# Kernel tuning notes

Hardware: AMD Instinct MI355X
Metric: run time of the kernel (lower is better)

Reference implementation:

```python
import jax, jax.numpy as jnp
import numpy as np

N = 50000      # nodes
E = 800000     # edges (avg degree 16)
D_IN = 128
HID = 128
OUT = 64


def setup_inputs() -> dict:
    key = jax.random.key(0)
    ks = jax.random.split(key, 10)
    s = 0.05
    return {
        "node_feats": jax.random.normal(ks[0], (N, D_IN), jnp.float32),
        "edge_index": jax.random.randint(ks[1], (2, E), 0, N, jnp.int32),
        "W1": jax.random.normal(ks[2], (D_IN, HID), jnp.float32) * s,
        "b1": jnp.zeros((HID,), jnp.float32),
        "W2": jax.random.normal(ks[3], (HID, HID), jnp.float32) * s,
        "b2": jnp.zeros((HID,), jnp.float32),
        "W3": jax.random.normal(ks[4], (HID, OUT), jnp.float32) * s,
        "b3": jnp.zeros((OUT,), jnp.float32),
        "skip_W": jax.random.normal(ks[5], (HID, OUT), jnp.float32) * s,
        "skip_b": jnp.zeros((OUT,), jnp.float32),
    }


def _gcn(h, src, dst, out_norm, in_norm, W, b):
    # DGL GraphConv, norm='both': scale src by out_deg^-1/2, sum over incoming
    # edges at dst, scale by in_deg^-1/2, then linear transform + bias.
    h = h * out_norm[:, None]                                   # [N, d]
    agg = jax.ops.segment_sum(h[src], dst, num_segments=N)      # [N, d]
    return (agg * in_norm[:, None]) @ W + b


def reference(node_feats, edge_index, W1, b1, W2, b2, W3, b3, skip_W, skip_b):
    src, dst = edge_index[0], edge_index[1]
    ones = jnp.ones((E,), jnp.float32)
    out_deg = jax.ops.segment_sum(ones, src, num_segments=N)
    in_deg = jax.ops.segment_sum(ones, dst, num_segments=N)
    out_norm = jnp.maximum(out_deg, 1.0) ** -0.5
    in_norm = jnp.maximum(in_deg, 1.0) ** -0.5

    # layer 0 (no skip) + ReLU
    h = jax.nn.relu(_gcn(node_feats, src, dst, out_norm, in_norm, W1, b1))
    # layer 1: same-dim residual blend + ReLU
    g2 = _gcn(h, src, dst, out_norm, in_norm, W2, b2)
    h = jax.nn.relu(0.6 * h + 0.4 * g2)
    # layer 2 (last, no ReLU): dims differ -> projected skip blend
    g3 = _gcn(h, src, dst, out_norm, in_norm, W3, b3)
    h = 0.6 * (h @ skip_W + skip_b) + 0.4 * g3
    return h[None]  # [1, N, OUT]
```

## Files before the change

kernel.cpp:

```cpp
#include <hip/hip_runtime.h>
#include <hip/hip_fp16.h>
#include <math.h>

#define TPB 256
#define CAP 64

__global__ __launch_bounds__(TPB) void k_count(const int* __restrict__ ei, int E,
                                               int* __restrict__ cnt, int* __restrict__ od,
                                               unsigned short* __restrict__ slots) {
    int t = blockIdx.x * TPB + threadIdx.x;
    int base = t * 4;
    if (base + 3 < E) {
        int4 s4 = *(const int4*)(ei + base);
        int4 d4 = *(const int4*)(ei + E + base);
        int p0 = atomicAdd(&cnt[d4.x], 1);
        int p1 = atomicAdd(&cnt[d4.y], 1);
        int p2 = atomicAdd(&cnt[d4.z], 1);
        int p3 = atomicAdd(&cnt[d4.w], 1);
        atomicAdd(&od[s4.x], 1);
        atomicAdd(&od[s4.y], 1);
        atomicAdd(&od[s4.z], 1);
        atomicAdd(&od[s4.w], 1);
        if (p0 < CAP) slots[(d4.x << 6) + p0] = (unsigned short)s4.x;
        if (p1 < CAP) slots[(d4.y << 6) + p1] = (unsigned short)s4.y;
        if (p2 < CAP) slots[(d4.z << 6) + p2] = (unsigned short)s4.z;
        if (p3 < CAP) slots[(d4.w << 6) + p3] = (unsigned short)s4.w;
    } else {
        for (int e = base; e < E; ++e) {
            int s = ei[e], d = ei[E + e];
            int pos = atomicAdd(&cnt[d], 1);
            if (pos < CAP) slots[(d << 6) + pos] = (unsigned short)s;
            atomicAdd(&od[s], 1);
        }
    }
}

__global__ __launch_bounds__(TPB) void k_norm(const int* __restrict__ od, const int* __restrict__ cnt,
                                              float* __restrict__ onr, float* __restrict__ rsq,
                                              float* __restrict__ inr, int N) {
    int i = blockIdx.x * TPB + threadIdx.x;
    if (i < N) {
        float o = fmaxf((float)od[i], 1.0f);
        float q = sqrtf(o);
        onr[i] = 1.0f / q;
        rsq[i] = q;
        inr[i] = 1.0f / sqrtf(fmaxf((float)cnt[i], 1.0f));
    }
}

__global__ __launch_bounds__(TPB) void k_cvt(const float* __restrict__ x, const float* __restrict__ onr,
                                             __half2* __restrict__ xh, int nF4) {
    int i4 = blockIdx.x * TPB + threadIdx.x;
    if (i4 >= nF4) return;
    int row = i4 >> 5;
    float on = onr[row];
    float4 v = ((const float4*)x)[i4];
    __half2 a = __floats2half2_rn(v.x * on, v.y * on);
    __half2 b = __floats2half2_rn(v.z * on, v.w * on);
    uint2 u;
    u.x = *reinterpret_cast<unsigned int*>(&a);
    u.y = *reinterpret_cast<unsigned int*>(&b);
    ((uint2*)xh)[i4] = u;
}

__global__ __launch_bounds__(TPB) void k_spmmh(const __half2* __restrict__ hp,
                                               const int* __restrict__ cnt,
                                               const unsigned short* __restrict__ slots,
                                               const float* __restrict__ inr,
                                               float* __restrict__ agg, int N) {
    int lane = threadIdx.x & 63;
    int r = blockIdx.x * 4 + (threadIdx.x >> 6);
    if (r >= N) return;
    int n = cnt[r]; if (n > CAP) n = CAP;
    const unsigned short* sl = slots + (r << 6);
    float ax0 = 0.f, ay0 = 0.f, ax1 = 0.f, ay1 = 0.f;
    float ax2 = 0.f, ay2 = 0.f, ax3 = 0.f, ay3 = 0.f;
    int e = 0;
    for (; e + 7 < n; e += 8) {
        ushort4 qa = *(const ushort4*)(sl + e);
        ushort4 qb = *(const ushort4*)(sl + e + 4);
        __half2 v0 = hp[qa.x * 64 + lane];
        __half2 v1 = hp[qa.y * 64 + lane];
        __half2 v2 = hp[qa.z * 64 + lane];
        __half2 v3 = hp[qa.w * 64 + lane];
        __half2 v4 = hp[qb.x * 64 + lane];
        __half2 v5 = hp[qb.y * 64 + lane];
        __half2 v6 = hp[qb.z * 64 + lane];
        __half2 v7 = hp[qb.w * 64 + lane];
        float2 f0 = __half22float2(v0), f1 = __half22float2(v1);
        float2 f2 = __half22float2(v2), f3 = __half22float2(v3);
        float2 f4 = __half22float2(v4), f5 = __half22float2(v5);
        float2 f6 = __half22float2(v6), f7 = __half22float2(v7);
        ax0 += f0.x + f1.x;  ay0 += f0.y + f1.y;
        ax1 += f2.x + f3.x;  ay1 += f2.y + f3.y;
        ax2 += f4.x + f5.x;  ay2 += f4.y + f5.y;
        ax3 += f6.x + f7.x;  ay3 += f6.y + f7.y;
    }
    for (; e + 3 < n; e += 4) {
        ushort4 qa = *(const ushort4*)(sl + e);
        float2 f0 = __half22float2(hp[qa.x * 64 + lane]);
        float2 f1 = __half22float2(hp[qa.y * 64 + lane]);
        float2 f2 = __half22float2(hp[qa.z * 64 + lane]);
        float2 f3 = __half22float2(hp[qa.w * 64 + lane]);
        ax0 += f0.x + f1.x;  ay0 += f0.y + f1.y;
        ax1 += f2.x + f3.x;  ay1 += f2.y + f3.y;
    }
    for (; e < n; ++e) {
        float2 f0 = __half22float2(hp[sl[e] * 64 + lane]);
        ax0 += f0.x;  ay0 += f0.y;
    }
    float sc = inr[r];
    float2 o;
    o.x = sc * ((ax0 + ax1) + (ax2 + ax3));
    o.y = sc * ((ay0 + ay1) + (ay2 + ay3));
    ((float2*)agg)[r * 64 + lane] = o;
}

__global__ __launch_bounds__(TPB) void k_spmm_final(const float* __restrict__ Pskip,
                                                    const __half* __restrict__ Ph,
                                                    const int* __restrict__ cnt,
                                                    const unsigned short* __restrict__ slots,
                                                    const float* __restrict__ inr,
                                                    const float* __restrict__ b3, const float* __restrict__ bs,
                                                    float* __restrict__ out, int N) {
    int lane = threadIdx.x & 63;
    int r = blockIdx.x * 4 + (threadIdx.x >> 6);
    if (r >= N) return;
    int n = cnt[r]; if (n > CAP) n = CAP;
    const unsigned short* sl = slots + (r << 6);
    float a0 = 0.f, a1 = 0.f, a2 = 0.f, a3 = 0.f;
    float a4 = 0.f, a5 = 0.f, a6 = 0.f, a7 = 0.f;
    int e = 0;
    for (; e + 7 < n; e += 8) {
        ushort4 qa = *(const ushort4*)(sl + e);
        ushort4 qb = *(const ushort4*)(sl + e + 4);
        a0 += __half2float(Ph[qa.x * 64 + lane]);
        a1 += __half2float(Ph[qa.y * 64 + lane]);
        a2 += __half2float(Ph[qa.z * 64 + lane]);
        a3 += __half2float(Ph[qa.w * 64 + lane]);
        a4 += __half2float(Ph[qb.x * 64 + lane]);
        a5 += __half2float(Ph[qb.y * 64 + lane]);
        a6 += __half2float(Ph[qb.z * 64 + lane]);
        a7 += __half2float(Ph[qb.w * 64 + lane]);
    }
    for (; e + 3 < n; e += 4) {
        ushort4 qa = *(const ushort4*)(sl + e);
        a0 += __half2float(Ph[qa.x * 64 + lane]);
        a1 += __half2float(Ph[qa.y * 64 + lane]);
        a2 += __half2float(Ph[qa.z * 64 + lane]);
        a3 += __half2float(Ph[qa.w * 64 + lane]);
    }
    for (; e < n; ++e) a0 += __half2float(Ph[sl[e] * 64 + lane]);
    float g3 = inr[r] * (((a0 + a1) + (a2 + a3)) + ((a4 + a5) + (a6 + a7))) + b3[lane];
    float skip = Pskip[r * 64 + lane] + bs[lane];
    out[r * 64 + lane] = 0.6f * skip + 0.4f * g3;
}

template <int MODE>
__global__ __launch_bounds__(TPB) void k_gemm(const float* __restrict__ A,
                                              const float* __restrict__ Wa, const float* __restrict__ Wb,
                                              const float* __restrict__ bias, const float* __restrict__ H,
                                              const float* __restrict__ onr, const float* __restrict__ rsq,
                                              float* __restrict__ C, __half* __restrict__ Ch, int N) {
    __shared__ float As[64][132];
    int t = threadIdx.x;
    int bm = blockIdx.x * 64;
#pragma unroll
    for (int rep = 0; rep < 8; ++rep) {
        int idx = rep * TPB + t;
        int i = idx >> 5;
        int k4 = (idx & 31) * 4;
        int row = bm + i;
        float4 v = make_float4(0.f, 0.f, 0.f, 0.f);
        if (row < N) {
            v = *(const float4*)(&A[row * 128 + k4]);
            if (MODE == 2) {
                float rs = rsq[row];
                v.x *= rs; v.y *= rs; v.z *= rs; v.w *= rs;
            }
        }
        *(float4*)(&As[i][k4]) = v;
    }
    __syncthreads();
    int tx = t & 31, ty = t >> 5;
    int j0 = tx * 4;
    const float* Wp;
    int jj, ldw;
    if (MODE == 2) { Wp = (j0 < 64) ? Wa : Wb; jj = j0 & 63; ldw = 64; }
    else           { Wp = Wa;                   jj = j0;      ldw = 128; }
    float4 acc[8];
#pragma unroll
    for (int q = 0; q < 8; ++q) acc[q] = make_float4(0.f, 0.f, 0.f, 0.f);
    for (int k = 0; k < 128; k += 4) {
        float4 w0 = *(const float4*)(&Wp[(k + 0) * ldw + jj]);
        float4 w1 = *(const float4*)(&Wp[(k + 1) * ldw + jj]);
        float4 w2 = *(const float4*)(&Wp[(k + 2) * ldw + jj]);
        float4 w3 = *(const float4*)(&Wp[(k + 3) * ldw + jj]);
#pragma unroll
        for (int q = 0; q < 8; ++q) {
            float4 a = *(const float4*)(&As[ty + 8 * q][k]);
            acc[q].x += a.x * w0.x + a.y * w1.x + a.z * w2.x + a.w * w3.x;
            acc[q].y += a.x * w0.y + a.y * w1.y + a.z * w2.y + a.w * w3.y;
            acc[q].z += a.x * w0.z + a.y * w1.z + a.z * w2.z + a.w * w3.z;
            acc[q].w += a.x * w0.w + a.y * w1.w + a.z * w2.w + a.w * w3.w;
        }
    }
    float4 bv = make_float4(0.f, 0.f, 0.f, 0.f);
    if (MODE != 2) bv = *(const float4*)(&bias[j0]);
#pragma unroll
    for (int q = 0; q < 8; ++q) {
        int row = bm + ty + 8 * q;
        if (row >= N) continue;
        float4 o;
        o.x = acc[q].x + bv.x;
        o.y = acc[q].y + bv.y;
        o.z = acc[q].z + bv.z;
        o.w = acc[q].w + bv.w;
        if (MODE == 1) {
            float hs = rsq[row];
            float4 h = *(const float4*)(&H[row * 128 + j0]);
            o.x = 0.6f * h.x * hs + 0.4f * o.x;
            o.y = 0.6f * h.y * hs + 0.4f * o.y;
            o.z = 0.6f * h.z * hs + 0.4f * o.z;
            o.w = 0.6f * h.w * hs + 0.4f * o.w;
        }
        if (MODE != 2) {
            float on = onr[row];
            o.x = fmaxf(o.x, 0.f) * on;
            o.y = fmaxf(o.y, 0.f) * on;
            o.z = fmaxf(o.z, 0.f) * on;
            o.w = fmaxf(o.w, 0.f) * on;
            *(float4*)(&C[row * 128 + j0]) = o;
            if (MODE == 0) {
                __half2 ha = __floats2half2_rn(o.x, o.y);
                __half2 hb = __floats2half2_rn(o.z, o.w);
                uint2 u;
                u.x = *reinterpret_cast<unsigned int*>(&ha);
                u.y = *reinterpret_cast<unsigned int*>(&hb);
                *(uint2*)(&Ch[row * 128 + j0]) = u;
            }
        } else {
            if (j0 < 64) {
                *(float4*)(&C[row * 64 + j0]) = o;
            } else {
                float on = onr[row];
                __half2 ha = __floats2half2_rn(o.x * on, o.y * on);
                __half2 hb = __floats2half2_rn(o.z * on, o.w * on);
                uint2 u;
                u.x = *reinterpret_cast<unsigned int*>(&ha);
                u.y = *reinterpret_cast<unsigned int*>(&hb);
                *(uint2*)(&Ch[row * 64 + (j0 - 64)]) = u;
            }
        }
    }
}

extern "C" void kernel_launch(void* const* d_in, const int* in_sizes, int n_in,
                              void* d_out, int out_size, void* d_ws, size_t ws_size,
                              hipStream_t stream) {
    const float* x  = (const float*)d_in[0];
    const int*   ei = (const int*)d_in[1];
    const float* W1 = (const float*)d_in[2];
    const float* b1 = (const float*)d_in[3];
    const float* W2 = (const float*)d_in[4];
    const float* b2 = (const float*)d_in[5];
    const float* W3 = (const float*)d_in[6];
    const float* b3 = (const float*)d_in[7];
    const float* Ws = (const float*)d_in[8];
    const float* bs = (const float*)d_in[9];
    float* out = (float*)d_out;

    int N = in_sizes[0] / 128;
    int E = in_sizes[1] / 2;

    char* p = (char*)d_ws;
    auto alloc = [&](size_t bytes) -> char* {
        char* r = p;
        p += (bytes + 255) & ~(size_t)255;
        return r;
    };
    size_t npad = ((size_t)N * 4 + 255) & ~(size_t)255;
    int*   cnt  = (int*)alloc(npad);
    int*   od   = (int*)alloc(npad);
    float* onr  = (float*)alloc((size_t)N * 4);
    float* rsq  = (float*)alloc((size_t)N * 4);
    float* inr  = (float*)alloc((size_t)N * 4);
    unsigned short* slots = (unsigned short*)alloc((size_t)N * CAP * 2);
    __half* xh  = (__half*)alloc((size_t)N * 128 * 2);
    float* agg  = (float*)alloc((size_t)N * 128 * 4);
    float* h1s  = (float*)alloc((size_t)N * 128 * 4);
    float* h2s  = (float*)alloc((size_t)N * 128 * 4);
    (void)ws_size; (void)n_in; (void)out_size;

    __half* h1h   = xh;
    float*  Pskip = agg;
    __half* Ph    = (__half*)(agg + (size_t)N * 64);

    int cBlocks = ((E + 3) / 4 + TPB - 1) / TPB;
    int nBlocks = (N + TPB - 1) / TPB;
    int cvtBlocks = (N * 32 + TPB - 1) / TPB;
    int spmmBlocks = (N + 3) / 4;
    int gemmBlocks = (N + 63) / 64;

    hipMemsetAsync(cnt, 0, npad * 2, stream);

    k_count<<<cBlocks, TPB, 0, stream>>>(ei, E, cnt, od, slots);
    k_norm<<<nBlocks, TPB, 0, stream>>>(od, cnt, onr, rsq, inr, N);
    k_cvt<<<cvtBlocks, TPB, 0, stream>>>(x, onr, (__half2*)xh, N * 32);

    k_spmmh<<<spmmBlocks, TPB, 0, stream>>>((const __half2*)xh, cnt, slots, inr, agg, N);
    k_gemm<0><<<gemmBlocks, TPB, 0, stream>>>(agg, W1, nullptr, b1, nullptr, onr, rsq, h1s, h1h, N);
    k_spmmh<<<spmmBlocks, TPB, 0, stream>>>((const __half2*)h1h, cnt, slots, inr, agg, N);
    k_gemm<1><<<gemmBlocks, TPB, 0, stream>>>(agg, W2, nullptr, b2, h1s, onr, rsq, h2s, nullptr, N);
    k_gemm<2><<<gemmBlocks, TPB, 0, stream>>>(h2s, Ws, W3, nullptr, nullptr, onr, rsq, Pskip, Ph, N);
    k_spmm_final<<<spmmBlocks, TPB, 0, stream>>>(Pskip, Ph, cnt, slots, inr, b3, bs, out, N);
}
```

Measured before the change: 376.4 us.

## Switch dense GEMMs to fp16 MFMA and store aggregates in half precision

Replaces the three fp32 FMA-based dense GEMMs with fp16 MFMA 16x16x32 instructions, using weights pre-transposed and converted to half by a new small kernel. The SpMM now writes its aggregate in half precision and layer-two activations are kept only in half, which halves intermediate memory traffic. The rsq rescaling path is removed in favour of storing unscaled fp32 h1 for the residual. This lowers GEMM compute and bandwidth costs but adds fp16 rounding on aggregates and activations.

Measured after the change: 334.5 us. -11.1%, faster.

```diff
diff --git a/kernel.cpp b/kernel.cpp
--- a/kernel.cpp
+++ b/kernel.cpp
@@ -4,6 +4,9 @@
 
 #define TPB 256
 #define CAP 64
+
+typedef _Float16 f16x8 __attribute__((ext_vector_type(8)));
+typedef float f32x4 __attribute__((ext_vector_type(4)));
 
 __global__ __launch_bounds__(TPB) void k_count(const int* __restrict__ ei, int E,
                                                int* __restrict__ cnt, int* __restrict__ od,
@@ -36,16 +39,28 @@
 }
 
 __global__ __launch_bounds__(TPB) void k_norm(const int* __restrict__ od, const int* __restrict__ cnt,
-                                              float* __restrict__ onr, float* __restrict__ rsq,
-                                              float* __restrict__ inr, int N) {
+                                              float* __restrict__ onr, float* __restrict__ inr, int N) {
     int i = blockIdx.x * TPB + threadIdx.x;
     if (i < N) {
-        float o = fmaxf((float)od[i], 1.0f);
-        float q = sqrtf(o);
-        onr[i] = 1.0f / q;
-        rsq[i] = q;
+        onr[i] = 1.0f / sqrtf(fmaxf((float)od[i], 1.0f));
         inr[i] = 1.0f / sqrtf(fmaxf((float)cnt[i], 1.0f));
     }
+}
+
+__global__ __launch_bounds__(TPB) void k_cvtw(const float* __restrict__ W1, const float* __restrict__ W2,
+                                              const float* __restrict__ Ws, const float* __restrict__ W3,
+                                              __half* __restrict__ W1T, __half* __restrict__ W2T,
+                                              __half* __restrict__ WCT) {
+    int idx = blockIdx.x * TPB + threadIdx.x;
+    int m = idx >> 14;
+    int r = idx & 16383;
+    int j = r >> 7, k = r & 127;
+    float v;
+    __half* dst;
+    if (m == 0)      { v = W1[k * 128 + j]; dst = W1T; }
+    else if (m == 1) { v = W2[k * 128 + j]; dst = W2T; }
+    else             { v = (j < 64) ? Ws[k * 64 + j] : W3[k * 64 + (j - 64)]; dst = WCT; }
+    dst[r] = __float2half(v);
 }
 
 __global__ __launch_bounds__(TPB) void k_cvt(const float* __restrict__ x, const float* __restrict__ onr,
@@ -67,7 +82,7 @@
                                                const int* __restrict__ cnt,
                                                const unsigned short* __restrict__ slots,
                                                const float* __restrict__ inr,
-                                               float* __restrict__ agg, int N) {
+                                               __half2* __restrict__ aggh, int N) {
     int lane = threadIdx.x & 63;
     int r = blockIdx.x * 4 + (threadIdx.x >> 6);
     if (r >= N) return;
@@ -79,18 +94,14 @@
     for (; e + 7 < n; e += 8) {
         ushort4 qa = *(const ushort4*)(sl + e);
         ushort4 qb = *(const ushort4*)(sl + e + 4);
-        __half2 v0 = hp[qa.x * 64 + lane];
-        __half2 v1 = hp[qa.y * 64 + lane];
-        __half2 v2 = hp[qa.z * 64 + lane];
-        __half2 v3 = hp[qa.w * 64 + lane];
-        __half2 v4 = hp[qb.x * 64 + lane];
-        __half2 v5 = hp[qb.y * 64 + lane];
-        __half2 v6 = hp[qb.z * 64 + lane];
-        __half2 v7 = hp[qb.w * 64 + lane];
-        float2 f0 = __half22float2(v0), f1 = __half22float2(v1);
-        float2 f2 = __half22float2(v2), f3 = __half22float2(v3);
-        float2 f4 = __half22float2(v4), f5 = __half22float2(v5);
-        float2 f6 = __half22float2(v6), f7 = __half22float2(v7);
+        float2 f0 = __half22float2(hp[qa.x * 64 + lane]);
+        float2 f1 = __half22float2(hp[qa.y * 64 + lane]);
+        float2 f2 = __half22float2(hp[qa.z * 64 + lane]);
+        float2 f3 = __half22float2(hp[qa.w * 64 + lane]);
+        float2 f4 = __half22float2(hp[qb.x * 64 + lane]);
+        float2 f5 = __half22float2(hp[qb.y * 64 + lane]);
+        float2 f6 = __half22float2(hp[qb.z * 64 + lane]);
+        float2 f7 = __half22float2(hp[qb.w * 64 + lane]);
         ax0 += f0.x + f1.x;  ay0 += f0.y + f1.y;
         ax1 += f2.x + f3.x;  ay1 += f2.y + f3.y;
         ax2 += f4.x + f5.x;  ay2 += f4.y + f5.y;
@@ -110,10 +121,8 @@
         ax0 += f0.x;  ay0 += f0.y;
     }
     float sc = inr[r];
-    float2 o;
-    o.x = sc * ((ax0 + ax1) + (ax2 + ax3));
-    o.y = sc * ((ay0 + ay1) + (ay2 + ay3));
-    ((float2*)agg)[r * 64 + lane] = o;
+    aggh[r * 64 + lane] =
+        __floats2half2_rn(sc * ((ax0 + ax1) + (ax2 + ax3)), sc * ((ay0 + ay1) + (ay2 + ay3)));
 }
 
 __global__ __launch_bounds__(TPB) void k_spmm_final(const float* __restrict__ Pskip,
@@ -157,99 +166,74 @@
 }
 
 template <int MODE>
-__global__ __launch_bounds__(TPB) void k_gemm(const float* __restrict__ A,
-                                              const float* __restrict__ Wa, const float* __restrict__ Wb,
-                                              const float* __restrict__ bias, const float* __restrict__ H,
-                                              const float* __restrict__ onr, const float* __restrict__ rsq,
-                                              float* __restrict__ C, __half* __restrict__ Ch, int N) {
-    __shared__ float As[64][132];
+__global__ __launch_bounds__(TPB) void k_mgemm(const __half* __restrict__ Ah,
+                                               const __half* __restrict__ WT,
+                                               const float* __restrict__ bias,
+                                               const float* __restrict__ Hres,
+                                               const float* __restrict__ onr,
+                                               float* __restrict__ Cf, __half* __restrict__ Chh,
+                                               int N) {
+    __shared__ _Float16 As[64][136];
     int t = threadIdx.x;
     int bm = blockIdx.x * 64;
 #pragma unroll
-    for (int rep = 0; rep < 8; ++rep) {
-        int idx = rep * TPB + t;
-        int i = idx >> 5;
-        int k4 = (idx & 31) * 4;
-        int row = bm + i;
-        float4 v = make_float4(0.f, 0.f, 0.f, 0.f);
-        if (row < N) {
-            v = *(const float4*)(&A[row * 128 + k4]);
-            if (MODE == 2) {
-                float rs = rsq[row];
-                v.x *= rs; v.y *= rs; v.z *= rs; v.w *= rs;
-            }
+    for (int rep = 0; rep < 4; ++rep) {
+        int c = rep * TPB + t;
+        int row = c >> 4, cc = c & 15;
+        int grow = bm + row;
+        f16x8 v = {0, 0, 0, 0, 0, 0, 0, 0};
+        if (grow < N) v = *(const f16x8*)(Ah + (size_t)grow * 128 + cc * 8);
+        *(f16x8*)(&As[row][cc * 8]) = v;
+    }
+    __syncthreads();
+    int l = t & 63;
+    int w = t >> 6;
+    int wrow = w * 16;
+    int lr = l & 15;
+    int lk = (l >> 4) * 8;
+    f32x4 acc[8];
+    f32x4 zero = {0.f, 0.f, 0.f, 0.f};
+#pragma unroll
+    for (int j = 0; j < 8; ++j) acc[j] = zero;
+#pragma unroll
+    for (int kk = 0; kk < 4; ++kk) {
+        f16x8 af = *(const f16x8*)(&As[wrow + lr][kk * 32 + lk]);
+#pragma unroll
+        for (int jt = 0; jt < 8; ++jt) {
+            f16x8 bf = *(const f16x8*)(WT + (size_t)(jt * 16 + lr) * 128 + kk * 32 + lk);
+            acc[jt] = __builtin_amdgcn_mfma_f32_16x16x32_f16(af, bf, acc[jt], 0, 0, 0);
         }
-        *(float4*)(&As[i][k4]) = v;
-    }
-    __syncthreads();
-    int tx = t & 31, ty = t >> 5;
-    int j0 = tx * 4;
-    const float* Wp;
-    int jj, ldw;
-    if (MODE == 2) { Wp = (j0 < 64) ? Wa : Wb; jj = j0 & 63; ldw = 64; }
-    else           { Wp = Wa;                   jj = j0;      ldw = 128; }
-    float4 acc[8];
-#pragma unroll
-    for (int q = 0; q < 8; ++q) acc[q] = make_float4(0.f, 0.f, 0.f, 0.f);
-    for (int k = 0; k < 128; k += 4) {
-        float4 w0 = *(const float4*)(&Wp[(k + 0) * ldw + jj]);
-        float4 w1 = *(const float4*)(&Wp[(k + 1) * ldw + jj]);
-        float4 w2 = *(const float4*)(&Wp[(k + 2) * ldw + jj]);
-        float4 w3 = *(const float4*)(&Wp[(k + 3) * ldw + jj]);
-#pragma unroll
-        for (int q = 0; q < 8; ++q) {
-            float4 a = *(const float4*)(&As[ty + 8 * q][k]);
-            acc[q].x += a.x * w0.x + a.y * w1.x + a.z * w2.x + a.w * w3.x;
-            acc[q].y += a.x * w0.y + a.y * w1.y + a.z * w2.y + a.w * w3.y;
-            acc[q].z += a.x * w0.z + a.y * w1.z + a.z * w2.z + a.w * w3.z;
-            acc[q].w += a.x * w0.w + a.y * w1.w + a.z * w2.w + a.w * w3.w;
+    }
+    int r0 = (l >> 4) * 4;
+    float onr4[4];
+    if (MODE == 0 || MODE == 2) {
+#pragma unroll
+        for (int r = 0; r < 4; ++r) {
+            int row = bm + wrow + r0 + r;
+            onr4[r] = (row < N) ? onr[row] : 0.f;
         }
     }
-    float4 bv = make_float4(0.f, 0.f, 0.f, 0.f);
-    if (MODE != 2) bv = *(const float4*)(&bias[j0]);
-#pragma unroll
-    for (int q = 0; q < 8; ++q) {
-        int row = bm + ty + 8 * q;
-        if (row >= N) continue;
-        float4 o;
-        o.x = acc[q].x + bv.x;
-        o.y = acc[q].y + bv.y;
-        o.z = acc[q].z + bv.z;
-        o.w = acc[q].w + bv.w;
-        if (MODE == 1) {
-            float hs = rsq[row];
-            float4 h = *(const float4*)(&H[row * 128 + j0]);
-            o.x = 0.6f * h.x * hs + 0.4f * o.x;
-            o.y = 0.6f * h.y * hs + 0.4f * o.y;
-            o.z = 0.6f * h.z * hs + 0.4f * o.z;
-            o.w = 0.6f * h.w * hs + 0.4f * o.w;
-        }
-        if (MODE != 2) {
-            float on = onr[row];
-            o.x = fmaxf(o.x, 0.f) * on;
-            o.y = fmaxf(o.y, 0.f) * on;
-            o.z = fmaxf(o.z, 0.f) * on;
-            o.w = fmaxf(o.w, 0.f) * on;
-            *(float4*)(&C[row * 128 + j0]) = o;
+#pragma unroll
+    for (int jt = 0; jt < 8; ++jt) {
+        int col = jt * 16 + lr;
+        float bv = 0.f;
+        if (MODE != 2) bv = bias[col];
+#pragma unroll
+        for (int r = 0; r < 4; ++r) {
+            int row = bm + wrow + r0 + r;
+            if (row >= N) continue;
+            float v = acc[jt][r] + bv;
             if (MODE == 0) {
-                __half2 ha = __floats2half2_rn(o.x, o.y);
-                __half2 hb = __floats2half2_rn(o.z, o.w);
-                uint2 u;
-                u.x = *reinterpret_cast<unsigned int*>(&ha);
-                u.y = *reinterpret_cast<unsigned int*>(&hb);
-                *(uint2*)(&Ch[row * 128 + j0]) = u;
-            }
-        } else {
-            if (j0 < 64) {
-                *(float4*)(&C[row * 64 + j0]) = o;
+                v = fmaxf(v, 0.f);
+                Cf[(size_t)row * 128 + col] = v;
+                Chh[(size_t)row * 128 + col] = __float2half(v * onr4[r]);
+            } else if (MODE == 1) {
+                float h1 = Hres[(size_t)row * 128 + col];
+                v = fmaxf(0.6f * h1 + 0.4f * v, 0.f);
+                Chh[(size_t)row * 128 + col] = __float2half(v);
             } else {
-                float on = onr[row];
-                __half2 ha = __floats2half2_rn(o.x * on, o.y * on);
-                __half2 hb = __floats2half2_rn(o.z * on, o.w * on);
-                uint2 u;
-                u.x = *reinterpret_cast<unsigned int*>(&ha);
-                u.y = *reinterpret_cast<unsigned int*>(&hb);
-                *(uint2*)(&Ch[row * 64 + (j0 - 64)]) = u;
+                if (jt < 4) Cf[(size_t)row * 64 + col] = v;
+                else        Chh[(size_t)row * 64 + (col - 64)] = __float2half(v * onr4[r]);
             }
         }
     }
@@ -283,35 +267,38 @@
     int*   cnt  = (int*)alloc(npad);
     int*   od   = (int*)alloc(npad);
     float* onr  = (float*)alloc((size_t)N * 4);
-    float* rsq  = (float*)alloc((size_t)N * 4);
     float* inr  = (float*)alloc((size_t)N * 4);
+    __half* W1T = (__half*)alloc(128 * 128 * 2);
+    __half* W2T = (__half*)alloc(128 * 128 * 2);
+    __half* WCT = (__half*)alloc(128 * 128 * 2);
     unsigned short* slots = (unsigned short*)alloc((size_t)N * CAP * 2);
-    __half* xh  = (__half*)alloc((size_t)N * 128 * 2);
-    float* agg  = (float*)alloc((size_t)N * 128 * 4);
-    float* h1s  = (float*)alloc((size_t)N * 128 * 4);
-    float* h2s  = (float*)alloc((size_t)N * 128 * 4);
+    __half* xh   = (__half*)alloc((size_t)N * 128 * 2);
+    __half* aggh = (__half*)alloc((size_t)N * 128 * 2);
+    float*  h1s  = (float*)alloc((size_t)N * 128 * 4);
+    __half* h1h  = (__half*)alloc((size_t)N * 128 * 2);
     (void)ws_size; (void)n_in; (void)out_size;
 
-    __half* h1h   = xh;
-    float*  Pskip = agg;
-    __half* Ph    = (__half*)(agg + (size_t)N * 64);
+    float*  Pskip = (float*)xh;
+    __half* Ph    = (__half*)aggh;
+    __half* h2h   = h1h;
 
     int cBlocks = ((E + 3) / 4 + TPB - 1) / TPB;
     int nBlocks = (N + TPB - 1) / TPB;
     int cvtBlocks = (N * 32 + TPB - 1) / TPB;
     int spmmBlocks = (N + 3) / 4;
-    int gemmBlocks = (N + 63) / 64;
+    int mgemmBlocks = (N + 63) / 64;
 
     hipMemsetAsync(cnt, 0, npad * 2, stream);
 
     k_count<<<cBlocks, TPB, 0, stream>>>(ei, E, cnt, od, slots);
-    k_norm<<<nBlocks, TPB, 0, stream>>>(od, cnt, onr, rsq, inr, N);
+    k_norm<<<nBlocks, TPB, 0, stream>>>(od, cnt, onr, inr, N);
+    k_cvtw<<<192, TPB, 0, stream>>>(W1, W2, Ws, W3, W1T, W2T, WCT);
     k_cvt<<<cvtBlocks, TPB, 0, stream>>>(x, onr, (__half2*)xh, N * 32);
 
-    k_spmmh<<<spmmBlocks, TPB, 0, stream>>>((const __half2*)xh, cnt, slots, inr, agg, N);
-    k_gemm<0><<<gemmBlocks, TPB, 0, stream>>>(agg, W1, nullptr, b1, nullptr, onr, rsq, h1s, h1h, N);
-    k_spmmh<<<spmmBlocks, TPB, 0, stream>>>((const __half2*)h1h, cnt, slots, inr, agg, N);
-    k_gemm<1><<<gemmBlocks, TPB, 0, stream>>>(agg, W2, nullptr, b2, h1s, onr, rsq, h2s, nullptr, N);
-    k_gemm<2><<<gemmBlocks, TPB, 0, stream>>>(h2s, Ws, W3, nullptr, nullptr, onr, rsq, Pskip, Ph, N);
+    k_spmmh<<<spmmBlocks, TPB, 0, stream>>>((const __half2*)xh, cnt, slots, inr, (__half2*)aggh, N);
+    k_mgemm<0><<<mgemmBlocks, TPB, 0, stream>>>(aggh, W1T, b1, nullptr, onr, h1s, h1h, N);
+    k_spmmh<<<spmmBlocks, TPB, 0, stream>>>((const __half2*)h1h, cnt, slots, inr, (__half2*)aggh, N);
+    k_mgemm<1><<<mgemmBlocks, TPB, 0, stream>>>(aggh, W2T, b2, h1s, onr, nullptr, h2h, N);
+    k_mgemm<2><<<mgemmBlocks, TPB, 0, stream>>>(h2h, WCT, nullptr, nullptr, onr, Pskip, Ph, N);
     k_spmm_final<<<spmmBlocks, TPB, 0, stream>>>(Pskip, Ph, cnt, slots, inr, b3, bs, out, N);
 }
```
